# Performance work log

Measured on AMD Instinct MI355X. Metric: run time of the kernel, lower is better.

Reference implementation:

```python
import jax, jax.numpy as jnp
import numpy as np

N = 100_000   # num nodes
E = 1_000_000 # num edges
F = 64        # feat_dim
H = 64        # hidden_dim
D = 64        # embed_dim


def _xavier(key, shape):
    limit = float(np.sqrt(6.0 / (shape[0] + shape[1])))
    return jax.random.uniform(key, shape, jnp.float32, -limit, limit)


def setup_inputs() -> dict:
    key = jax.random.key(0)
    ks = jax.random.split(key, 8)
    x = jax.random.normal(ks[0], (N, F), jnp.float32)
    edge_index = jax.random.randint(ks[1], (2, E), 0, N, dtype=jnp.int64)
    # GCNConv weights stored [in, out] (torch Linear transposed); biases zero-init
    return {
        "x": x,
        "edge_index": edge_index,
        "W1": _xavier(ks[2], (F, H)), "b1": jnp.zeros((H,), jnp.float32),
        "W2": _xavier(ks[3], (H, H)), "b2": jnp.zeros((H,), jnp.float32),
        "W3": _xavier(ks[4], (H, D)), "b3": jnp.zeros((D,), jnp.float32),
        "fw1": _xavier(ks[5], (D, H)), "fb1": jnp.zeros((H,), jnp.float32),
        "fw2": _xavier(ks[6], (H, D)), "fb2": jnp.zeros((D,), jnp.float32),
    }


def _gcn_conv(x, src, dst, dinv, W, b):
    # GCNConv: out = D^{-1/2} (A+I) D^{-1/2} (x W) + b
    h = x @ W                                   # [N, out]
    norm = dinv[src] * dinv[dst]                # [E]
    msg = h[src] * norm[:, None]                # gather + scale: [E, out]
    agg = jax.ops.segment_sum(msg, dst, num_segments=N)
    agg = agg + h * (dinv * dinv)[:, None]      # self-loop term
    return agg + b


def reference(x, edge_index, W1, b1, W2, b2, W3, b3, fw1, fb1, fw2, fb2):
    src, dst = edge_index[0], edge_index[1]
    # degree with self-loops (symmetric normalization)
    deg = jax.ops.segment_sum(jnp.ones((E,), x.dtype), dst, num_segments=N) + 1.0
    dinv = jax.lax.rsqrt(deg)
    # eval mode: dropout(p=0.5, training=False) is identity
    h = jax.nn.relu(_gcn_conv(x, src, dst, dinv, W1, b1))
    h = jax.nn.relu(_gcn_conv(h, src, dst, dinv, W2, b2))
    h = jax.nn.relu(_gcn_conv(h, src, dst, dinv, W3, b3))
    h = jax.nn.relu(h @ fw1 + fb1)
    return h @ fw2 + fb2                        # node embeddings [N, D]
```

## Files before the change

### kernel.cpp

```cpp
#include <hip/hip_runtime.h>
#include <cstdint>
#include <cstddef>


#define CDIV(a, b) (((a) + (b) - 1) / (b))

typedef __attribute__((ext_vector_type(8))) short bf16x8;
typedef __attribute__((ext_vector_type(4))) float f32x4;

static constexpr int BKT_SHIFT = 10;
static constexpr int BKT_NODES = 1 << BKT_SHIFT;
static constexpr int BKT_CAP = 13312;

__device__ __forceinline__ void split_bf(float a, short& hi, short& lo) {
  unsigned u = __float_as_uint(a);
  unsigned r = u + (0x7FFF + ((u >> 16) & 1));
  hi = (short)(r >> 16);
  float hirec = __uint_as_float(r & 0xFFFF0000u);
  float res = a - hirec;
  lo = (short)(__float_as_uint(res) >> 16);
}

__device__ __forceinline__ unsigned short f2bf_rne(float a) {
  unsigned u = __float_as_uint(a);
  u += 0x7FFF + ((u >> 16) & 1);
  return (unsigned short)(u >> 16);
}

__device__ __forceinline__ float4 bf4_to_f4(uint2 u) {
  float4 v;
  v.x = __uint_as_float(u.x << 16);
  v.y = __uint_as_float(u.x & 0xFFFF0000u);
  v.z = __uint_as_float(u.y << 16);
  v.w = __uint_as_float(u.y & 0xFFFF0000u);
  return v;
}

__device__ __forceinline__ void split8(float4 x, float4 y, bf16x8& h, bf16x8& l) {
  float av[8] = {x.x, x.y, x.z, x.w, y.x, y.y, y.z, y.w};
#pragma unroll
  for (int j = 0; j < 8; ++j) {
    short hi, lo;
    split_bf(av[j], hi, lo);
    h[j] = hi;
    l[j] = lo;
  }
}

__device__ __forceinline__ float4 nt_ld4(const float* p) {
  f32x4 v = __builtin_nontemporal_load(reinterpret_cast<const f32x4*>(p));
  float4 r;
  r.x = v[0]; r.y = v[1]; r.z = v[2]; r.w = v[3];
  return r;
}

__global__ void k_zero_i32(int* __restrict__ p, int n) {
  int i = blockIdx.x * blockDim.x + threadIdx.x;
  if (i < n) p[i] = 0;
}

__global__ __launch_bounds__(256)
void k_bucket(const int* __restrict__ ei, int* __restrict__ bcnt,
              int2* __restrict__ pairs, int E) {
  __shared__ int hist[128], rbase[128], roff[128];
  int t = threadIdx.x;
  int chunk = (E + gridDim.x - 1) / gridDim.x;
  int e0 = blockIdx.x * chunk;
  int e1 = min(e0 + chunk, E);
  if (t < 128) hist[t] = 0;
  __syncthreads();
  for (int e = e0 + t; e < e1; e += 256) {
    int d = __builtin_nontemporal_load(&ei[E + e]);
    atomicAdd(&hist[d >> BKT_SHIFT], 1);
  }
  __syncthreads();
  if (t < 128) {
    roff[t] = 0;
    rbase[t] = hist[t] ? atomicAdd(&bcnt[t], hist[t]) : 0;
  }
  __syncthreads();
  for (int e = e0 + t; e < e1; e += 256) {
    int d = __builtin_nontemporal_load(&ei[E + e]);
    int s = __builtin_nontemporal_load(&ei[e]);
    int b = d >> BKT_SHIFT;
    int r = atomicAdd(&roff[b], 1);
    int idx = rbase[b] + r;
    if (idx < BKT_CAP) pairs[(size_t)b * BKT_CAP + idx] = make_int2(s, d);
  }
}

__global__ __launch_bounds__(1024)
void k_build(const int2* __restrict__ pairs, const int* __restrict__ bcnt,
             int* __restrict__ row_ptr, float* __restrict__ dinv,
             int* __restrict__ srcs, int N, int E, int K) {
  __shared__ int cnt[BKT_NODES];
  __shared__ int deg[BKT_NODES];
  __shared__ int ebase_sh;
  int b = blockIdx.x;
  int t = threadIdx.x;
  int lo = b << BKT_SHIFT;
  int range = min(BKT_NODES, N - lo);
  int sz = min(bcnt[b], BKT_CAP);
  if (t == 0) {
    int s = 0;
    for (int i = 0; i < b; ++i) s += bcnt[i];
    ebase_sh = s;
  }
  cnt[t] = 0;
  __syncthreads();
  int ebase = ebase_sh;
  const int2* pb = pairs + (size_t)b * BKT_CAP;
  for (int i = t; i < sz; i += 1024) {
    atomicAdd(&cnt[pb[i].y - lo], 1);
  }
  __syncthreads();
  deg[t] = cnt[t];
  __syncthreads();
  int offset = 1;
  for (int d2 = BKT_NODES / 2; d2 > 0; d2 >>= 1) {
    if (t < d2) {
      int ai = offset * (2 * t + 1) - 1;
      int bi = offset * (2 * t + 2) - 1;
      cnt[bi] += cnt[ai];
    }
    offset <<= 1;
    __syncthreads();
  }
  if (t == 0) cnt[BKT_NODES - 1] = 0;
  __syncthreads();
  for (int d2 = 1; d2 < BKT_NODES; d2 <<= 1) {
    offset >>= 1;
    if (t < d2) {
      int ai = offset * (2 * t + 1) - 1;
      int bi = offset * (2 * t + 2) - 1;
      int tmp = cnt[ai];
      cnt[ai] = cnt[bi];
      cnt[bi] += tmp;
    }
    __syncthreads();
  }
  if (t < range) {
    row_ptr[lo + t] = ebase + cnt[t];
    dinv[lo + t] = rsqrtf((float)deg[t] + 1.0f);
  }
  if (b == K - 1 && t == 0) row_ptr[N] = E;
  __syncthreads();
  for (int i = t; i < sz; i += 1024) {
    int2 p = pb[i];
    int pos = ebase + atomicAdd(&cnt[p.y - lo], 1);
    srcs[pos] = p.x;
  }
}

__global__ void k_prep(const float* __restrict__ w0, const float* __restrict__ w1,
                       const float* __restrict__ w2, const float* __restrict__ w3,
                       const float* __restrict__ w4, bf16x8* __restrict__ packed) {
  const float* W;
  switch (blockIdx.x) {
    case 0: W = w0; break;
    case 1: W = w1; break;
    case 2: W = w2; break;
    case 3: W = w3; break;
    default: W = w4; break;
  }
  int tid = threadIdx.x;
  int lane = tid & 63;
  int q = (tid >> 6) & 1;
  int t = tid >> 7;
  int col = lane & 15, quad = lane >> 4;
  bf16x8 hi8, lo8;
#pragma unroll
  for (int j = 0; j < 8; ++j) {
    int k = q * 32 + quad * 8 + j;
    short hi, lo;
    split_bf(W[k * 64 + t * 16 + col], hi, lo);
    hi8[j] = hi;
    lo8[j] = lo;
  }
  size_t base = (size_t)blockIdx.x * 1024 + ((t * 2 + q) * 2) * 64 + lane;
  packed[base] = hi8;
  packed[base + 64] = lo8;
}

__global__ __launch_bounds__(256, 4)
void k_mm(const float* __restrict__ in, const bf16x8* __restrict__ Wp,
          const float* __restrict__ dinv, unsigned short* __restrict__ out, int n) {
  int lane = threadIdx.x & 63;
  int col = lane & 15, quad = lane >> 4;
  int tile = (blockIdx.x * blockDim.x + threadIdx.x) >> 6;
  int ntiles = (n + 15) >> 4;
  if (tile >= ntiles) return;

  bf16x8 wh[4][2], wl[4][2];
#pragma unroll
  for (int t = 0; t < 4; ++t)
#pragma unroll
    for (int q = 0; q < 2; ++q) {
      wh[t][q] = Wp[((t * 2 + q) * 2) * 64 + lane];
      wl[t][q] = Wp[((t * 2 + q) * 2 + 1) * 64 + lane];
    }

  int row0 = tile << 4;
  int ar = row0 + col;
  if (ar > n - 1) ar = n - 1;
  const float* arow = in + (size_t)ar * 64 + quad * 8;
  float4 a0 = nt_ld4(arow), a1 = nt_ld4(arow + 4);
  float4 a2 = nt_ld4(arow + 32), a3 = nt_ld4(arow + 36);

  bf16x8 ah[2], al[2];
  split8(a0, a1, ah[0], al[0]);
  split8(a2, a3, ah[1], al[1]);

  f32x4 acc[4];
#pragma unroll
  for (int t = 0; t < 4; ++t) acc[t] = (f32x4){0.f, 0.f, 0.f, 0.f};
#pragma unroll
  for (int t = 0; t < 4; ++t)
#pragma unroll
    for (int q = 0; q < 2; ++q) {
      acc[t] = __builtin_amdgcn_mfma_f32_16x16x32_bf16(ah[q], wh[t][q], acc[t], 0, 0, 0);
      acc[t] = __builtin_amdgcn_mfma_f32_16x16x32_bf16(ah[q], wl[t][q], acc[t], 0, 0, 0);
      acc[t] = __builtin_amdgcn_mfma_f32_16x16x32_bf16(al[q], wh[t][q], acc[t], 0, 0, 0);
    }
  float dv[4];
#pragma unroll
  for (int r = 0; r < 4; ++r) {
    int row = row0 + quad * 4 + r;
    dv[r] = (row < n) ? dinv[row] : 0.0f;
  }
#pragma unroll
  for (int t = 0; t < 4; ++t)
#pragma unroll
    for (int r = 0; r < 4; ++r) {
      int row = row0 + quad * 4 + r;
      if (row < n) out[(size_t)row * 64 + t * 16 + col] = f2bf_rne(acc[t][r] * dv[r]);
    }
}

template <bool HEAD>
__global__ __launch_bounds__(256, 4)
void k_agg_mm(const unsigned short* __restrict__ hws, const float* __restrict__ dinv,
              const int* __restrict__ row_ptr, const int* __restrict__ srcs,
              const float* __restrict__ bagg,
              const bf16x8* __restrict__ Wp1, const float* __restrict__ b1p,
              const bf16x8* __restrict__ Wp2, const float* __restrict__ b2p,
              void* __restrict__ out, int n) {
  constexpr int LDP = 68;
  __shared__ float a_sh[16 * LDP];
  int tid = threadIdx.x;
  int g = tid >> 4;
  int fg = tid & 15;
  int row0 = blockIdx.x << 4;
  const uint2* hw2 = (const uint2*)hws;

  int node = row0 + g;
  bool valid = node < n;
  int nd = valid ? node : (n - 1);
  uint2 su = hw2[(size_t)nd * 16 + fg];
  int p0 = 0, p1 = 0;
  if (valid) {
    p0 = row_ptr[node];
    p1 = row_ptr[node + 1];
  }
  float4 acc = make_float4(0.f, 0.f, 0.f, 0.f);
  if (p0 < p1) {
    int s[8];
#pragma unroll
    for (int j = 0; j < 8; ++j) {
      int ij = p0 + j;
      ij = (ij < p1) ? ij : (p1 - 1);
      s[j] = __builtin_nontemporal_load(&srcs[ij]);
    }
    for (int p = p0; p < p1; p += 8) {
      uint2 u[8];
#pragma unroll
      for (int j = 0; j < 8; ++j) u[j] = hw2[(size_t)s[j] * 16 + fg];
      int pn = p + 8;
      if (pn < p1) {
#pragma unroll
        for (int j = 0; j < 8; ++j) {
          int ij = pn + j;
          ij = (ij < p1) ? ij : (p1 - 1);
          s[j] = __builtin_nontemporal_load(&srcs[ij]);
        }
      }
      float4 v0 = bf4_to_f4(u[0]);
      acc.x += v0.x;
      acc.y += v0.y;
      acc.z += v0.z;
      acc.w += v0.w;
#pragma unroll
      for (int j = 1; j < 8; ++j) {
        float m = (p + j < p1) ? 1.f : 0.f;
        float4 v = bf4_to_f4(u[j]);
        acc.x = fmaf(m, v.x, acc.x);
        acc.y = fmaf(m, v.y, acc.y);
        acc.z = fmaf(m, v.z, acc.z);
        acc.w = fmaf(m, v.w, acc.w);
      }
    }
  }
  {
    float di = valid ? dinv[node] : 0.f;
    float4 selfv = bf4_to_f4(su);
    float4 b4 = ((const float4*)bagg)[fg];
    float4 r = make_float4(0.f, 0.f, 0.f, 0.f);
    if (valid) {
      r.x = fmaxf(fmaf(di, acc.x + selfv.x, b4.x), 0.f);
      r.y = fmaxf(fmaf(di, acc.y + selfv.y, b4.y), 0.f);
      r.z = fmaxf(fmaf(di, acc.z + selfv.z, b4.z), 0.f);
      r.w = fmaxf(fmaf(di, acc.w + selfv.w, b4.w), 0.f);
    }
    *(float4*)&a_sh[g * LDP + (fg << 2)] = r;
  }
  __syncthreads();

  int lane = threadIdx.x & 63;
  int wave = threadIdx.x >> 6;
  int col = lane & 15, quad = lane >> 4;
  const float* arow = &a_sh[col * LDP + (quad << 3)];
  float4 a0 = *(const float4*)(arow);
  float4 a1 = *(const float4*)(arow + 4);
  float4 a2 = *(const float4*)(arow + 32);
  float4 a3 = *(const float4*)(arow + 36);
  bf16x8 ah[2], al[2];
  split8(a0, a1, ah[0], al[0]);
  split8(a2, a3, ah[1], al[1]);

  bf16x8 wh[2], wl[2];
#pragma unroll
  for (int q = 0; q < 2; ++q) {
    wh[q] = Wp1[((wave * 2 + q) * 2) * 64 + lane];
    wl[q] = Wp1[((wave * 2 + q) * 2 + 1) * 64 + lane];
  }
  f32x4 acc1 = (f32x4){0.f, 0.f, 0.f, 0.f};
#pragma unroll
  for (int q = 0; q < 2; ++q) {
    acc1 = __builtin_amdgcn_mfma_f32_16x16x32_bf16(ah[q], wh[q], acc1, 0, 0, 0);
    acc1 = __builtin_amdgcn_mfma_f32_16x16x32_bf16(ah[q], wl[q], acc1, 0, 0, 0);
    acc1 = __builtin_amdgcn_mfma_f32_16x16x32_bf16(al[q], wh[q], acc1, 0, 0, 0);
  }

  if constexpr (!HEAD) {
#pragma unroll
    for (int r = 0; r < 4; ++r) {
      int row = row0 + (quad << 2) + r;
      if (row < n) {
        ((unsigned short*)out)[(size_t)row * 64 + wave * 16 + col] =
            f2bf_rne(acc1[r] * dinv[row]);
      }
    }
  } else {
    __shared__ float h_sh[16 * LDP];
    float bv1 = b1p[wave * 16 + col];
#pragma unroll
    for (int r = 0; r < 4; ++r) {
      h_sh[((quad << 2) + r) * LDP + wave * 16 + col] = fmaxf(acc1[r] + bv1, 0.f);
    }
    __syncthreads();
    const float* hrow = &h_sh[col * LDP + (quad << 3)];
    float4 h0 = *(const float4*)(hrow);
    float4 h1 = *(const float4*)(hrow + 4);
    float4 h2 = *(const float4*)(hrow + 32);
    float4 h3 = *(const float4*)(hrow + 36);
    bf16x8 ah2[2], al2[2];
    split8(h0, h1, ah2[0], al2[0]);
    split8(h2, h3, ah2[1], al2[1]);
    bf16x8 wh2[2], wl2[2];
#pragma unroll
    for (int q = 0; q < 2; ++q) {
      wh2[q] = Wp2[((wave * 2 + q) * 2) * 64 + lane];
      wl2[q] = Wp2[((wave * 2 + q) * 2 + 1) * 64 + lane];
    }
    f32x4 acc2 = (f32x4){0.f, 0.f, 0.f, 0.f};
#pragma unroll
    for (int q = 0; q < 2; ++q) {
      acc2 = __builtin_amdgcn_mfma_f32_16x16x32_bf16(ah2[q], wh2[q], acc2, 0, 0, 0);
      acc2 = __builtin_amdgcn_mfma_f32_16x16x32_bf16(ah2[q], wl2[q], acc2, 0, 0, 0);
      acc2 = __builtin_amdgcn_mfma_f32_16x16x32_bf16(al2[q], wh2[q], acc2, 0, 0, 0);
    }
    float bv2 = b2p[wave * 16 + col];
#pragma unroll
    for (int r = 0; r < 4; ++r) {
      int row = row0 + (quad << 2) + r;
      if (row < n) {
        ((float*)out)[(size_t)row * 64 + wave * 16 + col] = acc2[r] + bv2;
      }
    }
  }
}

extern "C" void kernel_launch(void* const* d_in, const int* in_sizes, int n_in,
                              void* d_out, int out_size, void* d_ws, size_t ws_size,
                              hipStream_t stream) {
  const float* x = (const float*)d_in[0];
  const int* ei = (const int*)d_in[1];
  const float* W1 = (const float*)d_in[2];
  const float* b1 = (const float*)d_in[3];
  const float* W2 = (const float*)d_in[4];
  const float* b2 = (const float*)d_in[5];
  const float* W3 = (const float*)d_in[6];
  const float* b3 = (const float*)d_in[7];
  const float* fw1 = (const float*)d_in[8];
  const float* fb1 = (const float*)d_in[9];
  const float* fw2 = (const float*)d_in[10];
  const float* fb2 = (const float*)d_in[11];
  float* out = (float*)d_out;

  const int N = in_sizes[0] / 64;
  const int E = in_sizes[1] / 2;
  const int K = CDIV(N, BKT_NODES);

  char* w = (char*)d_ws;
  auto take = [&](size_t bytes) -> char* {
    char* p = w;
    w += (bytes + 255) & ~(size_t)255;
    return p;
  };
  float* dinv = (float*)take((size_t)N * 4);
  int* row_ptr = (int*)take((size_t)(N + 1) * 4);
  int* bcnt = (int*)take((size_t)128 * 4);
  int* srcs = (int*)take((size_t)E * 4);
  bf16x8* wpack = (bf16x8*)take((size_t)5 * 1024 * 16);
  unsigned short* hwsA = (unsigned short*)take((size_t)N * 64 * 2);
  unsigned short* hwsB = (unsigned short*)take((size_t)N * 64 * 2);
  int2* pairs = (int2*)hwsA;

  const int B = 256;

  k_prep<<<5, 512, 0, stream>>>(W1, W2, W3, fw1, fw2, wpack);
  k_zero_i32<<<1, 128, 0, stream>>>(bcnt, 128);
  k_bucket<<<256, B, 0, stream>>>(ei, bcnt, pairs, E);
  k_build<<<K, 1024, 0, stream>>>(pairs, bcnt, row_ptr, dinv, srcs, N, E, K);

  const int ntiles = CDIV(N, 16);
  const int MMG = CDIV(ntiles, 4);

  k_mm<<<MMG, B, 0, stream>>>(x, wpack + 0 * 1024, dinv, hwsA, N);
  k_agg_mm<false><<<ntiles, B, 0, stream>>>(hwsA, dinv, row_ptr, srcs, b1,
                                            wpack + 1 * 1024, nullptr, nullptr, nullptr,
                                            hwsB, N);
  k_agg_mm<false><<<ntiles, B, 0, stream>>>(hwsB, dinv, row_ptr, srcs, b2,
                                            wpack + 2 * 1024, nullptr, nullptr, nullptr,
                                            hwsA, N);
  k_agg_mm<true><<<ntiles, B, 0, stream>>>(hwsA, dinv, row_ptr, srcs, b3,
                                           wpack + 3 * 1024, fb1, wpack + 4 * 1024, fb2,
                                           out, N);
}
```

Before: 255.7 us.

## Fold bucket-count zeroing into prep, add zero sentinel row, widen bucket grid

Moves the bucket-counter zeroing into an extra block of the weight-prep kernel, removing one kernel launch. Adds a zeroed sentinel row at index N in the intermediate feature buffers so out-of-range neighbor slots gather zeros, which replaces the masked FMA accumulation with plain adds. Also raises the bucketing grid from 256 to 1024 blocks and reuses the aggregation shared buffer for the head MLP, at the cost of an extra barrier. The sentinel row is written by the producer kernels and adds one row to each buffer.

```diff
diff --git a/kernel.cpp b/kernel.cpp
--- a/kernel.cpp
+++ b/kernel.cpp
@@ -52,11 +52,6 @@
   float4 r;
   r.x = v[0]; r.y = v[1]; r.z = v[2]; r.w = v[3];
   return r;
-}
-
-__global__ void k_zero_i32(int* __restrict__ p, int n) {
-  int i = blockIdx.x * blockDim.x + threadIdx.x;
-  if (i < n) p[i] = 0;
 }
 
 __global__ __launch_bounds__(256)
@@ -154,7 +149,12 @@
 
 __global__ void k_prep(const float* __restrict__ w0, const float* __restrict__ w1,
                        const float* __restrict__ w2, const float* __restrict__ w3,
-                       const float* __restrict__ w4, bf16x8* __restrict__ packed) {
+                       const float* __restrict__ w4, bf16x8* __restrict__ packed,
+                       int* __restrict__ bcnt) {
+  if (blockIdx.x == 5) {
+    if (threadIdx.x < 128) bcnt[threadIdx.x] = 0;
+    return;
+  }
   const float* W;
   switch (blockIdx.x) {
     case 0: W = w0; break;
@@ -185,6 +185,9 @@
 __global__ __launch_bounds__(256, 4)
 void k_mm(const float* __restrict__ in, const bf16x8* __restrict__ Wp,
           const float* __restrict__ dinv, unsigned short* __restrict__ out, int n) {
+  if (blockIdx.x == 0 && threadIdx.x < 32) {
+    ((unsigned int*)out)[(size_t)n * 32 + threadIdx.x] = 0u;
+  }
   int lane = threadIdx.x & 63;
   int col = lane & 15, quad = lane >> 4;
   int tile = (blockIdx.x * blockDim.x + threadIdx.x) >> 6;
@@ -253,10 +256,15 @@
   int row0 = blockIdx.x << 4;
   const uint2* hw2 = (const uint2*)hws;
 
+  if (!HEAD && blockIdx.x == 0 && tid < 32) {
+    ((unsigned int*)out)[(size_t)n * 32 + tid] = 0u;
+  }
+
   int node = row0 + g;
   bool valid = node < n;
-  int nd = valid ? node : (n - 1);
+  int nd = valid ? node : n;
   uint2 su = hw2[(size_t)nd * 16 + fg];
+  float di = valid ? dinv[node] : 0.f;
   int p0 = 0, p1 = 0;
   if (valid) {
     p0 = row_ptr[node];
@@ -268,8 +276,9 @@
 #pragma unroll
     for (int j = 0; j < 8; ++j) {
       int ij = p0 + j;
-      ij = (ij < p1) ? ij : (p1 - 1);
-      s[j] = __builtin_nontemporal_load(&srcs[ij]);
+      bool ok = ij < p1;
+      int sv = __builtin_nontemporal_load(&srcs[ok ? ij : p1 - 1]);
+      s[j] = ok ? sv : n;
     }
     for (int p = p0; p < p1; p += 8) {
       uint2 u[8];
@@ -280,28 +289,22 @@
 #pragma unroll
         for (int j = 0; j < 8; ++j) {
           int ij = pn + j;
-          ij = (ij < p1) ? ij : (p1 - 1);
-          s[j] = __builtin_nontemporal_load(&srcs[ij]);
+          bool ok = ij < p1;
+          int sv = __builtin_nontemporal_load(&srcs[ok ? ij : p1 - 1]);
+          s[j] = ok ? sv : n;
         }
       }
-      float4 v0 = bf4_to_f4(u[0]);
-      acc.x += v0.x;
-      acc.y += v0.y;
-      acc.z += v0.z;
-      acc.w += v0.w;
-#pragma unroll
-      for (int j = 1; j < 8; ++j) {
-        float m = (p + j < p1) ? 1.f : 0.f;
+#pragma unroll
+      for (int j = 0; j < 8; ++j) {
         float4 v = bf4_to_f4(u[j]);
-        acc.x = fmaf(m, v.x, acc.x);
-        acc.y = fmaf(m, v.y, acc.y);
-        acc.z = fmaf(m, v.z, acc.z);
-        acc.w = fmaf(m, v.w, acc.w);
+        acc.x += v.x;
+        acc.y += v.y;
+        acc.z += v.z;
+        acc.w += v.w;
       }
     }
   }
   {
-    float di = valid ? dinv[node] : 0.f;
     float4 selfv = bf4_to_f4(su);
     float4 b4 = ((const float4*)bagg)[fg];
     float4 r = make_float4(0.f, 0.f, 0.f, 0.f);
@@ -315,8 +318,8 @@
   }
   __syncthreads();
 
-  int lane = threadIdx.x & 63;
-  int wave = threadIdx.x >> 6;
+  int lane = tid & 63;
+  int wave = tid >> 6;
   int col = lane & 15, quad = lane >> 4;
   const float* arow = &a_sh[col * LDP + (quad << 3)];
   float4 a0 = *(const float4*)(arow);
@@ -351,14 +354,14 @@
       }
     }
   } else {
-    __shared__ float h_sh[16 * LDP];
     float bv1 = b1p[wave * 16 + col];
+    __syncthreads();
 #pragma unroll
     for (int r = 0; r < 4; ++r) {
-      h_sh[((quad << 2) + r) * LDP + wave * 16 + col] = fmaxf(acc1[r] + bv1, 0.f);
+      a_sh[((quad << 2) + r) * LDP + wave * 16 + col] = fmaxf(acc1[r] + bv1, 0.f);
     }
     __syncthreads();
-    const float* hrow = &h_sh[col * LDP + (quad << 3)];
+    const float* hrow = &a_sh[col * LDP + (quad << 3)];
     float4 h0 = *(const float4*)(hrow);
     float4 h1 = *(const float4*)(hrow + 4);
     float4 h2 = *(const float4*)(hrow + 32);
@@ -422,15 +425,14 @@
   int* bcnt = (int*)take((size_t)128 * 4);
   int* srcs = (int*)take((size_t)E * 4);
   bf16x8* wpack = (bf16x8*)take((size_t)5 * 1024 * 16);
-  unsigned short* hwsA = (unsigned short*)take((size_t)N * 64 * 2);
-  unsigned short* hwsB = (unsigned short*)take((size_t)N * 64 * 2);
+  unsigned short* hwsA = (unsigned short*)take((size_t)(N + 1) * 64 * 2);
+  unsigned short* hwsB = (unsigned short*)take((size_t)(N + 1) * 64 * 2);
   int2* pairs = (int2*)hwsA;
 
   const int B = 256;
 
-  k_prep<<<5, 512, 0, stream>>>(W1, W2, W3, fw1, fw2, wpack);
-  k_zero_i32<<<1, 128, 0, stream>>>(bcnt, 128);
-  k_bucket<<<256, B, 0, stream>>>(ei, bcnt, pairs, E);
+  k_prep<<<6, 512, 0, stream>>>(W1, W2, W3, fw1, fw2, wpack, bcnt);
+  k_bucket<<<1024, B, 0, stream>>>(ei, bcnt, pairs, E);
   k_build<<<K, 1024, 0, stream>>>(pairs, bcnt, row_ptr, dinv, srcs, N, E, K);
 
   const int ntiles = CDIV(N, 16);
```

Result: no change. 260.0 us (+1.7%).
